# Kernel tuning notes

Measured on AMD Instinct MI355X. Metric: run time of the kernel, lower is better.

The kernel has to match this reference:

```python
import jax, jax.numpy as jnp
import numpy as np

PS = 8          # patch size
D_STATE = 16
D_CONV = 4
DT_RANK = 6     # ceil(96/16)
N_HEADS = 2
NEG = jnp.float32(-1e30)
_DIRS = np.array([[-1, 0], [1, 0], [0, -1], [0, 1]], np.int32)


def _ln(x, w, b, eps=1e-5):
    mu = x.mean(-1, keepdims=True)
    var = ((x - mu) ** 2).mean(-1, keepdims=True)
    return (x - mu) * jax.lax.rsqrt(var + eps) * w + b


def _vit_score_map(x, pos_embed, proj_w, proj_b, in_w, in_b, out_w, out_b,
                   ln1_w, ln1_b, ff1_w, ff1_b, ff2_w, ff2_b, ln2_w, ln2_b,
                   score_w, score_b):
    B, C, H, W = x.shape
    Hp, Wp = H // PS, W // PS
    N = Hp * Wp
    E = proj_w.shape[0]
    # F.unfold ordering: per patch the vector is (C, kr, kc) flattened
    patches = x.reshape(B, C, Hp, PS, Wp, PS).transpose(0, 2, 4, 1, 3, 5).reshape(B, N, C * PS * PS)
    patches = patches @ proj_w.T + proj_b
    if pos_embed.shape[1] != N:
        o = int(pos_embed.shape[1] ** 0.5)
        pe = jax.image.resize(pos_embed.reshape(1, o, o, E), (1, Hp, Wp, E), 'bilinear').reshape(1, N, E)
    else:
        pe = pos_embed
    patches = patches + 0.1 * pe
    # nn.TransformerEncoderLayer defaults: post-norm, ReLU, eval (no dropout)
    qkv = patches @ in_w.T + in_b
    q, k, v = jnp.split(qkv, 3, axis=-1)
    dh = E // N_HEADS
    def heads(t):
        return t.reshape(B, N, N_HEADS, dh).transpose(0, 2, 1, 3)
    q, k, v = heads(q), heads(k), heads(v)
    attn = jax.nn.softmax(jnp.einsum('bhqd,bhkd->bhqk', q, k) / np.float32(np.sqrt(dh)), axis=-1)
    ctx = jnp.einsum('bhqk,bhkd->bhqd', attn, v).transpose(0, 2, 1, 3).reshape(B, N, E)
    src = _ln(patches + (ctx @ out_w.T + out_b), ln1_w, ln1_b)
    ff = jax.nn.relu(src @ ff1_w.T + ff1_b) @ ff2_w.T + ff2_b
    src = _ln(src + ff, ln2_w, ln2_b)
    scores = jax.nn.sigmoid((src @ score_w.T + score_b)[..., 0])
    pvar = patches.var(axis=-1, ddof=1)          # torch.var is unbiased
    final = 0.7 * scores + 0.3 * jax.nn.sigmoid(pvar * 10.0)
    return final.reshape(B, Hp, Wp)


def _traversal(score):
    """Greedy adaptive patch traversal: start at global argmax, walk to the best
    unvisited 4-neighbor; on dead-end jump to the global argmax over unvisited."""
    Hp, Wp = score.shape
    n = Hp * Wp
    s = score.reshape(-1)
    dirs = jnp.asarray(_DIRS)
    start = jnp.argmax(s).astype(jnp.int32)
    visited0 = jnp.zeros((n,), bool).at[start].set(True)

    def step(carry, _):
        visited, cur = carry
        ci, cj = cur // Wp, cur % Wp
        ni, nj = ci + dirs[:, 0], cj + dirs[:, 1]
        valid = (ni >= 0) & (ni < Hp) & (nj >= 0) & (nj < Wp)
        nidx = (jnp.clip(ni, 0, Hp - 1) * Wp + jnp.clip(nj, 0, Wp - 1)).astype(jnp.int32)
        nsc = jnp.where(valid & ~visited[nidx], s[nidx], NEG)
        b = jnp.argmax(nsc)                       # first-max tie-break == '>' loop order
        jump = jnp.argmax(jnp.where(visited, NEG, s)).astype(jnp.int32)
        nxt = jnp.where(nsc[b] > NEG * 0.5, nidx[b], jump).astype(jnp.int32)
        return (visited.at[nxt].set(True), nxt), nxt

    _, rest = jax.lax.scan(step, (visited0, start), None, length=n - 1)
    return jnp.concatenate([start[None], rest])


def _mamba(u, in_w, conv_w, conv_b, xproj_w, dt_w, dt_b, A_log, D_skip, out_w):
    B, L, _ = u.shape
    d_in = conv_w.shape[0]
    xz = u @ in_w.T                               # (B,L,2*d_in)
    xx, z = jnp.split(xz, 2, axis=-1)
    # causal depthwise conv over sequence
    xc = jnp.pad(xx.transpose(0, 2, 1), ((0, 0), (0, 0), (D_CONV - 1, 0)))
    xc = jax.lax.conv_general_dilated(xc, conv_w, (1,), 'VALID',
                                      feature_group_count=d_in,
                                      dimension_numbers=('NCH', 'OIH', 'NCH'))
    xx = jax.nn.silu((xc + conv_b[None, :, None]).transpose(0, 2, 1))   # (B,L,d_in)
    dbl = xx @ xproj_w.T
    dt, Bm, Cm = jnp.split(dbl, [DT_RANK, DT_RANK + D_STATE], axis=-1)
    dt = jax.nn.softplus(dt @ dt_w.T + dt_b)      # (B,L,d_in)
    A = -jnp.exp(A_log)                           # (d_in, d_state)

    def step(h, inp):
        dt_t, B_t, C_t, x_t = inp                 # (B,d_in),(B,ds),(B,ds),(B,d_in)
        h = jnp.exp(dt_t[..., None] * A) * h + (dt_t * x_t)[..., None] * B_t[:, None, :]
        return h, jnp.einsum('bds,bs->bd', h, C_t)

    h0 = jnp.zeros((B, d_in, D_STATE), u.dtype)
    xs = (dt.transpose(1, 0, 2), Bm.transpose(1, 0, 2), Cm.transpose(1, 0, 2), xx.transpose(1, 0, 2))
    _, ys = jax.lax.scan(step, h0, xs)
    y = ys.transpose(1, 0, 2) + xx * D_skip
    return (y * jax.nn.silu(z)) @ out_w.T


def setup_inputs() -> dict:
    key = jax.random.key(0)
    ks = jax.random.split(key, 20)
    B, C, H, W = 2, 96, 128, 128
    E, FF = 96, 2048
    d_in, dr, ds, dc = 192, 6, 16, 4
    f32 = jnp.float32
    def w(k, shape, s=0.02):
        return jax.random.normal(k, shape, f32) * s
    return dict(
        x=jax.random.normal(ks[0], (B, C, H, W), f32),
        pe=w(ks[1], (B, H * W, C), 0.02),
        pos_embed=w(ks[2], (1, 784, E)),
        vit_proj_w=w(ks[3], (E, C * PS * PS)),
        vit_proj_b=jnp.zeros((E,), f32),
        attn_in_w=w(ks[4], (3 * E, E)),
        attn_in_b=jnp.zeros((3 * E,), f32),
        attn_out_w=w(ks[5], (E, E)),
        attn_out_b=jnp.zeros((E,), f32),
        ln1_w=jnp.ones((E,), f32), ln1_b=jnp.zeros((E,), f32),
        ff1_w=w(ks[6], (FF, E)), ff1_b=jnp.zeros((FF,), f32),
        ff2_w=w(ks[7], (E, FF)), ff2_b=jnp.zeros((E,), f32),
        ln2_w=jnp.ones((E,), f32), ln2_b=jnp.zeros((E,), f32),
        score_w=w(ks[8], (1, E)), score_b=jnp.zeros((1,), f32),
        norm_w=jnp.ones((C,), f32), norm_b=jnp.zeros((C,), f32),
        in_proj_w=w(ks[9], (2 * d_in, C)),
        conv_w=w(ks[10], (d_in, 1, dc), 0.1),
        conv_b=jnp.zeros((d_in,), f32),
        x_proj_w=w(ks[11], (dr + 2 * ds, d_in)),
        dt_w=w(ks[12], (d_in, dr)),
        dt_b=jnp.full((d_in,), -4.6, f32),        # softplus(dt_b) ~ 0.01 (mamba dt init)
        A_log=jnp.log(jnp.tile(jnp.arange(1, ds + 1, dtype=f32), (d_in, 1))),
        D_skip=jnp.ones((d_in,), f32),
        out_proj_w=w(ks[13], (C, d_in)),
    )


def reference(x, pe, pos_embed, vit_proj_w, vit_proj_b, attn_in_w, attn_in_b,
              attn_out_w, attn_out_b, ln1_w, ln1_b, ff1_w, ff1_b, ff2_w, ff2_b,
              ln2_w, ln2_b, score_w, score_b, norm_w, norm_b, in_proj_w,
              conv_w, conv_b, x_proj_w, dt_w, dt_b, A_log, D_skip, out_proj_w):
    B, C, H, W = x.shape
    n = H * W
    # Dynamic_Adaptive_Scan with the code's DCNv3Function-is-None fallback:
    # x = input_last, permuted back to channels-first => identity on x.
    x_adapted = x
    score_map = _vit_score_map(x_adapted, pos_embed, vit_proj_w, vit_proj_b,
                               attn_in_w, attn_in_b, attn_out_w, attn_out_b,
                               ln1_w, ln1_b, ff1_w, ff1_b, ff2_w, ff2_b,
                               ln2_w, ln2_b, score_w, score_b)
    order = jax.vmap(_traversal)(jax.lax.stop_gradient(score_map))    # (B, Hp*Wp)
    Hp, Wp = score_map.shape[1], score_map.shape[2]
    pi, pj = order // Wp, order % Wp
    # expand each patch into its PSxPS pixels in raster order
    offs = (jnp.arange(PS, dtype=jnp.int32)[:, None] * W + jnp.arange(PS, dtype=jnp.int32)[None, :]).reshape(-1)
    idx = ((pi * PS * W + pj * PS)[..., None] + offs).reshape(B, n)    # (B, n)
    x_tok = jnp.take_along_axis(x_adapted.reshape(B, C, n), idx[:, None, :], axis=2).transpose(0, 2, 1)
    pe_r = jnp.take_along_axis(pe, idx[..., None], axis=1)
    tokens = _ln(x_tok + pe_r, norm_w, norm_b)
    y = _mamba(tokens, in_proj_w, conv_w, conv_b, x_proj_w, dt_w, dt_b, A_log, D_skip, out_proj_w)
    # scatter back to spatial raster order
    out = jax.vmap(lambda yb, ib: jnp.zeros_like(yb).at[ib].set(yb))(y, idx)
    return out.transpose(0, 2, 1).reshape(B, C, H, W)
```

## Files before the change

### kernel.cpp

```cpp
#include <hip/hip_runtime.h>
#include <math.h>

#define BB 2
#define CC 96
#define HH 128
#define WW 128
#define PS 8
#define HP 16
#define WP 16
#define NPATCH 256
#define EE 96
#define FF 2048
#define DH 48
#define DIN 192
#define DR 6
#define DS 16
#define LL 16384
#define NCHUNK 512
#define CLEN 32
#define NSEG 16
#define SEGC 32
#define KTOT 6144
#define KSPLIT 32
#define KSL 192

__device__ __forceinline__ float sigmoid_acc(float x){ return 1.f/(1.f+expf(-x)); }
__device__ __forceinline__ float sigmoid_fast(float x){ return 1.f/(1.f+__expf(-x)); }

__global__ void k_resize_pe(const float* __restrict__ pos, float* __restrict__ pe16){
  int n = blockIdx.x;
  int oi = n / WP, oj = n % WP;
  int e = threadIdx.x;
  const float inv = 1.75f;
  float sfi = (oi + 0.5f)*inv - 0.5f;
  float sfj = (oj + 0.5f)*inv - 0.5f;
  int i0 = max(0, (int)ceilf(sfi - inv)), i1 = min(27, (int)floorf(sfi + inv));
  int j0 = max(0, (int)ceilf(sfj - inv)), j1 = min(27, (int)floorf(sfj + inv));
  float si = 0.f, sj = 0.f;
  for(int j=i0;j<=i1;j++) si += fmaxf(0.f, 1.f - fabsf(sfi - (float)j)/inv);
  for(int j=j0;j<=j1;j++) sj += fmaxf(0.f, 1.f - fabsf(sfj - (float)j)/inv);
  float acc = 0.f;
  for(int ji=i0;ji<=i1;ji++){
    float wv = fmaxf(0.f, 1.f - fabsf(sfi - (float)ji)/inv) / si;
    for(int jj=j0;jj<=j1;jj++){
      float wu = fmaxf(0.f, 1.f - fabsf(sfj - (float)jj)/inv);
      acc += wv * (wu/sj) * pos[(ji*28+jj)*EE + e];
    }
  }
  pe16[n*EE + e] = acc;
}

__global__ void k_wtr(const float* __restrict__ vw, float* __restrict__ Wt){
  __shared__ float t[64*97];
  int k0 = blockIdx.x*64;
  int tid = threadIdx.x;
  for(int i=tid;i<64*EE;i+=256){
    int e = i>>6, kk = i&63;
    t[kk*97 + e] = vw[(size_t)e*KTOT + k0 + kk];
  }
  __syncthreads();
  for(int i=tid;i<64*EE;i+=256){
    int kk = i/EE, e = i%EE;
    Wt[(size_t)(k0+kk)*EE + e] = t[kk*97 + e];
  }
}

__global__ __launch_bounds__(384) void k_pproj(const float* __restrict__ x,
    const float* __restrict__ Wt, float* __restrict__ part){
  __shared__ float As[16*196];
  int bidx = blockIdx.x;
  int ks = bidx & (KSPLIT-1);
  int pb = bidx >> 5;
  int b = pb >> 4, pi = pb & 15;
  int c0 = ks*3;
  int tid = threadIdx.x;
  for(int i=tid;i<24*128;i+=384){
    int row = i>>7;
    int col = i&127;
    int cl = row>>3, dr = row&7;
    float v = x[(((size_t)(b*CC + c0+cl))<<14) + (size_t)((pi*PS+dr)<<7) + col];
    As[(col>>3)*196 + cl*64 + dr*8 + (col&7)] = v;
  }
  __syncthreads();
  int e = tid % EE;
  int pq = tid / EE;
  const float* wp = Wt + (size_t)(ks*KSL)*EE + e;
  float acc0=0.f, acc1=0.f, acc2=0.f, acc3=0.f;
  const float4* A0 = (const float4*)(As + (pq*4+0)*196);
  const float4* A1 = (const float4*)(As + (pq*4+1)*196);
  const float4* A2 = (const float4*)(As + (pq*4+2)*196);
  const float4* A3 = (const float4*)(As + (pq*4+3)*196);
  #pragma unroll 4
  for(int k4=0;k4<48;k4++){
    float w0 = wp[(k4*4+0)*EE];
    float w1 = wp[(k4*4+1)*EE];
    float w2 = wp[(k4*4+2)*EE];
    float w3 = wp[(k4*4+3)*EE];
    float4 a;
    a = A0[k4]; acc0 += a.x*w0 + a.y*w1 + a.z*w2 + a.w*w3;
    a = A1[k4]; acc1 += a.x*w0 + a.y*w1 + a.z*w2 + a.w*w3;
    a = A2[k4]; acc2 += a.x*w0 + a.y*w1 + a.z*w2 + a.w*w3;
    a = A3[k4]; acc3 += a.x*w0 + a.y*w1 + a.z*w2 + a.w*w3;
  }
  size_t gp0 = (size_t)b*NPATCH + pi*WP + pq*4;
  part[((size_t)ks*512 + gp0+0)*EE + e] = acc0;
  part[((size_t)ks*512 + gp0+1)*EE + e] = acc1;
  part[((size_t)ks*512 + gp0+2)*EE + e] = acc2;
  part[((size_t)ks*512 + gp0+3)*EE + e] = acc3;
}

__global__ __launch_bounds__(320) void k_preduce_qkv(const float* __restrict__ part,
    const float* __restrict__ pb, const float* __restrict__ pe16,
    const float* __restrict__ inw, const float* __restrict__ inb,
    float* __restrict__ patches, float* __restrict__ pvar, float* __restrict__ qkv){
  int gp = blockIdx.x;
  int n = gp % NPATCH;
  int tid = threadIdx.x;
  __shared__ float a[EE];
  __shared__ float ps[2], pq2[2];
  float v = 0.f;
  if(tid < EE){
    float s = 0.f;
    #pragma unroll 8
    for(int ks=0;ks<KSPLIT;ks++) s += part[((size_t)ks*512 + gp)*EE + tid];
    v = s + pb[tid] + 0.1f*pe16[n*EE + tid];
    a[tid] = v;
    patches[(size_t)gp*EE + tid] = v;
  }
  if(tid < 128){
    float sv = v, sq = v*v;
    for(int off=32; off>0; off>>=1){ sv += __shfl_xor(sv, off); sq += __shfl_xor(sq, off); }
    if((tid&63)==0){ ps[tid>>6]=sv; pq2[tid>>6]=sq; }
  }
  __syncthreads();
  if(tid==0){
    float s = ps[0]+ps[1], qq = pq2[0]+pq2[1];
    float mu = s/EE;
    pvar[gp] = (qq - EE*mu*mu)/(EE-1);
  }
  if(tid < 288){
    const float4* ar = (const float4*)a;
    const float4* wr = (const float4*)(inw + (size_t)tid*EE);
    float4 s4 = {0.f,0.f,0.f,0.f};
    #pragma unroll
    for(int k=0;k<24;k++){
      float4 av=ar[k], wv=wr[k];
      s4.x += av.x*wv.x; s4.y += av.y*wv.y; s4.z += av.z*wv.z; s4.w += av.w*wv.w;
    }
    qkv[(size_t)gp*288 + tid] = inb[tid] + (s4.x+s4.y)+(s4.z+s4.w);
  }
}

__global__ void k_attn(const float* __restrict__ qkv, float* __restrict__ ctx){
  int gb = blockIdx.x;
  int i = gb % NPATCH; int h = (gb/NPATCH)&1; int b = gb/(NPATCH*2);
  int tid = threadIdx.x;
  __shared__ float q[DH];
  __shared__ float p[NPATCH];
  __shared__ float red[NPATCH];
  __shared__ float red2[4][DH];
  const float* base = qkv + (size_t)b*NPATCH*288;
  if(tid < DH) q[tid] = base[(size_t)i*288 + h*DH + tid];
  __syncthreads();
  float sc;
  {
    const float4* krow = (const float4*)(base + (size_t)tid*288 + 96 + h*DH);
    const float4* q4 = (const float4*)q;
    float4 s4 = {0.f,0.f,0.f,0.f};
    #pragma unroll
    for(int k=0;k<12;k++){
      float4 kv=krow[k], qv=q4[k];
      s4.x += qv.x*kv.x; s4.y += qv.y*kv.y; s4.z += qv.z*kv.z; s4.w += qv.w*kv.w;
    }
    sc = ((s4.x+s4.y)+(s4.z+s4.w)) * 0.14433756729740643f;
  }
  red[tid] = sc; __syncthreads();
  for(int st=128; st>0; st>>=1){ if(tid<st) red[tid]=fmaxf(red[tid],red[tid+st]); __syncthreads(); }
  float mx = red[0]; __syncthreads();
  float ev = expf(sc - mx);
  red[tid] = ev; __syncthreads();
  for(int st=128; st>0; st>>=1){ if(tid<st) red[tid]+=red[tid+st]; __syncthreads(); }
  float denom = red[0]; __syncthreads();
  p[tid] = ev/denom;
  __syncthreads();
  if(tid < 192){
    int jg = tid/DH, dd = tid%DH;
    const float* vb = base + 192 + h*DH + dd;
    float acc0 = 0.f, acc1 = 0.f;
    #pragma unroll 4
    for(int j=jg*64; j<jg*64+64; j+=2){
      acc0 += p[j]*vb[(size_t)j*288];
      acc1 += p[j+1]*vb[(size_t)(j+1)*288];
    }
    red2[jg][dd] = acc0+acc1;
  }
  __syncthreads();
  if(tid < DH){
    ctx[((size_t)b*NPATCH + i)*EE + h*DH + tid] =
      red2[0][tid]+red2[1][tid]+red2[2][tid]+red2[3][tid];
  }
}

__global__ void k_ln1(const float* __restrict__ ctx, const float* __restrict__ ow,
                      const float* __restrict__ ob, const float* __restrict__ patches,
                      const float* __restrict__ lw, const float* __restrict__ lb,
                      float* __restrict__ src1){
  int row = blockIdx.x; int tid = threadIdx.x;
  __shared__ float a[EE];
  __shared__ float ps[2], pq2[2], st[2];
  if(tid < EE) a[tid] = ctx[(size_t)row*EE + tid];
  __syncthreads();
  float o = 0.f;
  if(tid < EE){
    const float4* ar = (const float4*)a;
    const float4* wr = (const float4*)(ow + (size_t)tid*EE);
    float4 s4 = {0.f,0.f,0.f,0.f};
    #pragma unroll
    for(int k=0;k<24;k++){
      float4 av=ar[k], wv=wr[k];
      s4.x += av.x*wv.x; s4.y += av.y*wv.y; s4.z += av.z*wv.z; s4.w += av.w*wv.w;
    }
    o = ob[tid] + (s4.x+s4.y)+(s4.z+s4.w) + patches[(size_t)row*EE + tid];
  }
  float sv = o, sq = o*o;
  for(int off=32; off>0; off>>=1){ sv += __shfl_xor(sv, off); sq += __shfl_xor(sq, off); }
  if((tid&63)==0){ ps[tid>>6]=sv; pq2[tid>>6]=sq; }
  __syncthreads();
  if(tid==0){
    float s = ps[0]+ps[1], qq = pq2[0]+pq2[1];
    float mu = s/EE;
    st[0]=mu; st[1]=rsqrtf(qq/EE - mu*mu + 1e-5f);
  }
  __syncthreads();
  if(tid < EE) src1[(size_t)row*EE + tid] = (o-st[0])*st[1]*lw[tid] + lb[tid];
}

__global__ __launch_bounds__(512) void k_ff1(const float* __restrict__ src1,
    const float* __restrict__ w1, const float* __restrict__ b1, float* __restrict__ ffh){
  int row0 = blockIdx.x*2; int tid = threadIdx.x;
  const float4* a0 = (const float4*)(src1 + (size_t)row0*EE);
  const float4* a1 = (const float4*)(src1 + (size_t)(row0+1)*EE);
  for(int fo=0;fo<4;fo++){
    int f = fo*512 + tid;
    const float4* wr = (const float4*)(w1 + (size_t)f*EE);
    float bc = b1[f];
    float acc0=bc, acc1=bc;
    #pragma unroll
    for(int k=0;k<24;k++){
      float4 wv = wr[k];
      float4 av;
      av = a0[k]; acc0 += av.x*wv.x+av.y*wv.y+av.z*wv.z+av.w*wv.w;
      av = a1[k]; acc1 += av.x*wv.x+av.y*wv.y+av.z*wv.z+av.w*wv.w;
    }
    ffh[(size_t)(row0+0)*FF + f] = fmaxf(acc0, 0.f);
    ffh[(size_t)(row0+1)*FF + f] = fmaxf(acc1, 0.f);
  }
}

__global__ __launch_bounds__(384) void k_ff2(const float* __restrict__ ffh,
    const float* __restrict__ w2, const float* __restrict__ b2,
    const float* __restrict__ src1, float* __restrict__ src2){
  __shared__ float partl[8][EE];
  int row0 = blockIdx.x*2; int tid = threadIdx.x;
  int e = tid % EE, fg = tid / EE;
  const float4* wr = (const float4*)(w2 + (size_t)e*FF + fg*512);
  const float4* h0 = (const float4*)(ffh + (size_t)row0*FF + fg*512);
  const float4* h1 = (const float4*)(ffh + (size_t)(row0+1)*FF + fg*512);
  float acc0=0.f, acc1=0.f;
  #pragma unroll 4
  for(int k=0;k<128;k++){
    float4 wv = wr[k];
    float4 hv;
    hv = h0[k]; acc0 += hv.x*wv.x+hv.y*wv.y+hv.z*wv.z+hv.w*wv.w;
    hv = h1[k]; acc1 += hv.x*wv.x+hv.y*wv.y+hv.z*wv.z+hv.w*wv.w;
  }
  partl[0*4+fg][e] = acc0;
  partl[1*4+fg][e] = acc1;
  __syncthreads();
  if(tid < 192){
    int r = tid / EE, e2 = tid % EE;
    float s = partl[r*4+0][e2] + partl[r*4+1][e2] + partl[r*4+2][e2] + partl[r*4+3][e2];
    src2[(size_t)(row0+r)*EE + e2] = s + b2[e2] + src1[(size_t)(row0+r)*EE + e2];
  }
}

__global__ void k_ln2_score(const float* __restrict__ src2,
    const float* __restrict__ lw, const float* __restrict__ lb,
    const float* __restrict__ sw, const float* __restrict__ sb,
    const float* __restrict__ pvar, float* __restrict__ fscore){
  int row = blockIdx.x; int tid = threadIdx.x;
  float v = (tid < EE) ? src2[(size_t)row*EE + tid] : 0.f;
  float sv = v, sq = v*v;
  for(int off=32; off>0; off>>=1){ sv += __shfl_xor(sv, off); sq += __shfl_xor(sq, off); }
  __shared__ float ps[2], pq2[2], st[2];
  int wid = tid>>6;
  if((tid&63)==0){ ps[wid]=sv; pq2[wid]=sq; }
  __syncthreads();
  if(tid==0){
    float s = ps[0]+ps[1], qq = pq2[0]+pq2[1];
    float mu = s/EE;
    st[0]=mu; st[1]=rsqrtf(qq/EE - mu*mu + 1e-5f);
  }
  __syncthreads();
  float o = (tid < EE) ? ((v-st[0])*st[1]*lw[tid] + lb[tid]) * sw[tid] : 0.f;
  for(int off=32; off>0; off>>=1) o += __shfl_xor(o, off);
  if((tid&63)==0) ps[wid] = o;
  __syncthreads();
  if(tid==0){
    float acc = ps[0]+ps[1] + sb[0];
    fscore[row] = 0.7f*sigmoid_acc(acc) + 0.3f*sigmoid_acc(pvar[row]*10.f);
  }
}

__global__ void k_traversal(const float* __restrict__ fscore, int* __restrict__ order){
  int b = blockIdx.x; int lane = threadIdx.x;
  __shared__ float fsl[NPATCH];
  __shared__ int   sidxl[NPATCH];
  for(int k=lane;k<NPATCH;k+=64) fsl[k] = fscore[b*NPATCH+k];
  __syncthreads();
  {
    float s0=fsl[lane], s1=fsl[64+lane], s2=fsl[128+lane], s3=fsl[192+lane];
    int i0=lane, i1=64+lane, i2=128+lane, i3=192+lane;
    int c0=0,c1=0,c2=0,c3=0;
    for(int j=0;j<NPATCH;j++){
      float sj=fsl[j];
      c0 += (sj>s0 || (sj==s0 && j<i0)) ? 1:0;
      c1 += (sj>s1 || (sj==s1 && j<i1)) ? 1:0;
      c2 += (sj>s2 || (sj==s2 && j<i2)) ? 1:0;
      c3 += (sj>s3 || (sj==s3 && j<i3)) ? 1:0;
    }
    sidxl[c0]=i0; sidxl[c1]=i1; sidxl[c2]=i2; sidxl[c3]=i3;
  }
  __syncthreads();
  if(lane==0){
    int ptr = 0;
    int cur = sidxl[0];
    order[b*NPATCH] = cur;
    fsl[cur] = -1e30f;
    for(int step=1; step<NPATCH; step++){
      int ci = cur>>4, cj = cur&15;
      float n0 = (ci>0)  ? fsl[cur-16] : -1e30f;
      float n1 = (ci<15) ? fsl[cur+16] : -1e30f;
      float n2 = (cj>0)  ? fsl[cur-1]  : -1e30f;
      float n3 = (cj<15) ? fsl[cur+1]  : -1e30f;
      float bv = n0; int bi = cur-16;
      if(n1 > bv){ bv=n1; bi=cur+16; }
      if(n2 > bv){ bv=n2; bi=cur-1; }
      if(n3 > bv){ bv=n3; bi=cur+1; }
      int nxt;
      if(bv > -1e29f){
        nxt = bi;
      } else {
        while(fsl[sidxl[ptr]] <= -1e29f) ptr++;
        nxt = sidxl[ptr];
      }
      fsl[nxt] = -1e30f;
      order[b*NPATCH + step] = nxt;
      cur = nxt;
    }
  }
}

__global__ __launch_bounds__(256) void k_gather_ln(const float* __restrict__ x,
    const float* __restrict__ pe, const int* __restrict__ order,
    const float* __restrict__ nw, const float* __restrict__ nb,
    float* __restrict__ tokens){
  __shared__ float val[64*97];
  int gb = blockIdx.x; int b = gb >> 8; int r = gb & 255;
  int tid = threadIdx.x;
  int p = order[b*NPATCH + r]; int pi = p>>4, pj = p&15;
  for(int i=tid;i<96*64;i+=256){
    int c = i>>6, q = i&63;
    int dr = q>>3, dc = q&7;
    val[q*97 + c] = x[(((size_t)(b*CC + c))<<14) + (size_t)((pi*PS+dr)<<7) + pj*PS + dc];
  }
  __syncthreads();
  for(int i=tid;i<64*EE;i+=256){
    int q = i/EE, c = i%EE;
    int pix = ((pi*PS + (q>>3))<<7) + pj*PS + (q&7);
    val[q*97 + c] += pe[((size_t)b*(HH*WW) + pix)*CC + c];
  }
  __syncthreads();
  int wid = tid>>6, lane = tid&63;
  for(int t=wid; t<64; t+=4){
    float v1 = val[t*97 + lane];
    float v2 = (lane<32) ? val[t*97 + 64 + lane] : 0.f;
    float sv = v1+v2, sq = v1*v1 + v2*v2;
    for(int off=32; off>0; off>>=1){ sv += __shfl_xor(sv, off); sq += __shfl_xor(sq, off); }
    float mu = sv/EE;
    float rs = rsqrtf(sq/EE - mu*mu + 1e-5f);
    size_t tb = ((size_t)b*LL + r*64 + t)*EE;
    tokens[tb + lane] = (v1-mu)*rs*nw[lane] + nb[lane];
    if(lane < 32) tokens[tb + 64 + lane] = (v2-mu)*rs*nw[64+lane] + nb[64+lane];
  }
}

__global__ __launch_bounds__(768, 5) void k_inproj_conv(const float* __restrict__ tokens,
    const float* __restrict__ w, const float* __restrict__ cw, const float* __restrict__ cb,
    float* __restrict__ z, float* __restrict__ xc){
  __shared__ float a[35*EE];
  __shared__ float ps[12*384];
  __shared__ float xxl[35*DIN];
  int rb = blockIdx.x; size_t row0 = (size_t)rb*32;
  int l0 = (int)(row0 % LL);
  int tid = threadIdx.x;
  int kh = tid / 384;
  int col = tid - kh*384;
  {
    const float4* src = (const float4*)(tokens + (row0-3)*EE);
    float4* adst = (float4*)a;
    for(int idx=tid; idx<840; idx+=768){
      float4 v;
      if(l0==0 && idx<72){ v.x=0.f; v.y=0.f; v.z=0.f; v.w=0.f; }
      else v = src[idx];
      adst[idx] = v;
    }
  }
  float4 wv[12];
  const float4* wr4 = (const float4*)(w + (size_t)col*EE + kh*48);
  #pragma unroll
  for(int i=0;i<12;i++) wv[i] = wr4[i];
  __syncthreads();
  #pragma unroll
  for(int g=0; g<3; g++){
    float acc[12];
    #pragma unroll
    for(int r=0;r<12;r++){
      int gi = g*12 + r;
      if(gi < 35){
        const float4* ar = (const float4*)(a + gi*EE + kh*48);
        float4 s4 = {0.f,0.f,0.f,0.f};
        #pragma unroll
        for(int i=0;i<12;i++){
          float4 av = ar[i];
          s4.x += av.x*wv[i].x; s4.y += av.y*wv[i].y; s4.z += av.z*wv[i].z; s4.w += av.w*wv[i].w;
        }
        acc[r] = (s4.x+s4.y)+(s4.z+s4.w);
      } else acc[r] = 0.f;
    }
    if(kh==1){
      #pragma unroll
      for(int r=0;r<12;r++) if(g*12+r < 35) ps[r*384 + col] = acc[r];
    }
    __syncthreads();
    if(kh==0){
      #pragma unroll
      for(int r=0;r<12;r++){
        int gi = g*12 + r;
        if(gi < 35){
          float tot = acc[r] + ps[r*384 + col];
          if(col < DIN) xxl[gi*DIN + col] = tot;
          else if(gi >= 3) z[(row0 + gi - 3)*DIN + (col - DIN)] = tot;
        }
      }
    }
    __syncthreads();
  }
  #pragma unroll
  for(int it=0; it<8; it++){
    int idx = tid + it*768;
    int rr = idx / DIN, d = idx - rr*DIN;
    float v = cb[d]
      + cw[d*4+0]*xxl[(rr+0)*DIN + d]
      + cw[d*4+1]*xxl[(rr+1)*DIN + d]
      + cw[d*4+2]*xxl[(rr+2)*DIN + d]
      + cw[d*4+3]*xxl[(rr+3)*DIN + d];
    xc[(row0 + rr)*DIN + d] = v * sigmoid_fast(v);
  }
}

__global__ __launch_bounds__(320) void k_xproj(const float* __restrict__ xc, const float* __restrict__ xpw,
    const float* __restrict__ dtw, const float* __restrict__ dtb,
    float* __restrict__ dt, float* __restrict__ Bm, float* __restrict__ Cm){
  __shared__ float a[8][196];
  __shared__ float dbl[8][40];
  int rb = blockIdx.x; size_t row0 = (size_t)rb*8;
  int tid = threadIdx.x;
  for(int i=tid;i<8*DIN;i+=320){ int r=i/DIN, k=i%DIN; a[r][k] = xc[(row0+r)*DIN + k]; }
  __syncthreads();
  {
    int r = tid & 7, o = tid >> 3;
    if(o < 38){
      const float4* wr = (const float4*)(xpw + (size_t)o*DIN);
      const float4* ar = (const float4*)(a[r]);
      float4 s4 = {0.f,0.f,0.f,0.f};
      #pragma unroll
      for(int k=0;k<48;k++){
        float4 av=ar[k], wv=wr[k];
        s4.x += av.x*wv.x; s4.y += av.y*wv.y; s4.z += av.z*wv.z; s4.w += av.w*wv.w;
      }
      dbl[r][o] = (s4.x+s4.y)+(s4.z+s4.w);
    }
  }
  __syncthreads();
  for(int t=tid;t<8*DIN;t+=320){
    int r = t/DIN, d = t%DIN;
    float acc = dtb[d];
    #pragma unroll
    for(int j=0;j<DR;j++) acc += dbl[r][j]*dtw[d*DR+j];
    dt[(row0+r)*DIN + d] = fmaxf(acc, 0.f) + log1pf(__expf(-fabsf(acc)));
  }
  if(tid < 8*DS){
    int r = tid/DS, s = tid%DS;
    Bm[(row0+r)*DS + s] = dbl[r][6+s];
    Cm[(row0+r)*DS + s] = dbl[r][22+s];
  }
}

__global__ __launch_bounds__(192) void k_scan1(const float* __restrict__ dt,
    const float* __restrict__ xc, const float* __restrict__ Bm,
    const float* __restrict__ Alog, float* __restrict__ hend, float* __restrict__ sumdt){
  int blk = blockIdx.x;
  int b = blk >> 9, c = blk & (NCHUNK-1);
  int d = threadIdx.x;
  float A[16];
  {
    const float4* a4 = (const float4*)(Alog + d*DS);
    #pragma unroll
    for(int i=0;i<4;i++){
      float4 v = a4[i];
      A[i*4+0]=-expf(v.x); A[i*4+1]=-expf(v.y); A[i*4+2]=-expf(v.z); A[i*4+3]=-expf(v.w);
    }
  }
  float h[16];
  #pragma unroll
  for(int s=0;s<16;s++) h[s]=0.f;
  float sd = 0.f;
  size_t base = (size_t)b*LL + (size_t)c*CLEN;
  const float* dp = dt + base*DIN + d;
  const float* xp = xc + base*DIN + d;
  const float4* bp = (const float4*)(Bm + base*DS);
  for(int t=0;t<CLEN;t++){
    float dtv = dp[(size_t)t*DIN];
    float xv  = xp[(size_t)t*DIN];
    float4 b0=bp[t*4+0], b1=bp[t*4+1], b2=bp[t*4+2], b3=bp[t*4+3];
    float e[16];
    #pragma unroll
    for(int s=0;s<16;s++) e[s] = __expf(dtv*A[s]);
    float Bv[16] = {b0.x,b0.y,b0.z,b0.w,b1.x,b1.y,b1.z,b1.w,b2.x,b2.y,b2.z,b2.w,b3.x,b3.y,b3.z,b3.w};
    float dx = dtv*xv; sd += dtv;
    #pragma unroll
    for(int s=0;s<16;s++) h[s] = e[s]*h[s] + dx*Bv[s];
  }
  size_t o = ((size_t)c*BB + b)*DIN + d;
  float4* hp = (float4*)(hend + o*DS);
  hp[0] = make_float4(h[0],h[1],h[2],h[3]);
  hp[1] = make_float4(h[4],h[5],h[6],h[7]);
  hp[2] = make_float4(h[8],h[9],h[10],h[11]);
  hp[3] = make_float4(h[12],h[13],h[14],h[15]);
  sumdt[o] = sd;
}

__global__ __launch_bounds__(256) void k_scan2a(const float* __restrict__ hend,
    const float* __restrict__ sumdt, const float* __restrict__ Alog,
    float* __restrict__ segP, float* __restrict__ segH){
  int g = blockIdx.x*256 + threadIdx.x;
  int seg = g / 6144; int r = g % 6144;
  int b = r / 3072; int d = (r % 3072) >> 4; int s = r & 15;
  float A = -expf(Alog[d*DS + s]);
  float P = 1.f, H = 0.f;
  int c0 = seg*SEGC;
  for(int cc=0; cc<SEGC; cc+=4){
    float sd[4], he[4];
    #pragma unroll
    for(int j=0;j<4;j++){
      size_t o = ((size_t)(c0+cc+j)*BB + b)*DIN + d;
      sd[j] = sumdt[o]; he[j] = hend[o*DS + s];
    }
    #pragma unroll
    for(int j=0;j<4;j++){
      float aa = __expf(A*sd[j]);
      H = aa*H + he[j]; P *= aa;
    }
  }
  segP[seg*6144 + r] = P; segH[seg*6144 + r] = H;
}

__global__ void k_scan2b(const float* __restrict__ segP, const float* __restrict__ segH,
                         float* __restrict__ segHin){
  int r = blockIdx.x*256 + threadIdx.x;
  float P[NSEG], H[NSEG];
  #pragma unroll
  for(int sg=0; sg<NSEG; sg++){ P[sg]=segP[sg*6144+r]; H[sg]=segH[sg*6144+r]; }
  float h = 0.f;
  #pragma unroll
  for(int sg=0; sg<NSEG; sg++){
    segHin[sg*6144 + r] = h;
    h = P[sg]*h + H[sg];
  }
}

__global__ __launch_bounds__(256) void k_scan2c(float* __restrict__ hend,
    const float* __restrict__ sumdt, const float* __restrict__ Alog,
    const float* __restrict__ segHin){
  int g = blockIdx.x*256 + threadIdx.x;
  int seg = g / 6144; int r = g % 6144;
  int b = r / 3072; int d = (r % 3072) >> 4; int s = r & 15;
  float A = -expf(Alog[d*DS + s]);
  float h = segHin[seg*6144 + r];
  int c0 = seg*SEGC;
  for(int cc=0; cc<SEGC; cc+=4){
    float sd[4], he[4]; size_t oo[4];
    #pragma unroll
    for(int j=0;j<4;j++){
      oo[j] = ((size_t)(c0+cc+j)*BB + b)*DIN + d;
      sd[j] = sumdt[oo[j]]; he[j] = hend[oo[j]*DS + s];
    }
    #pragma unroll
    for(int j=0;j<4;j++){
      hend[oo[j]*DS + s] = h;
      float aa = __expf(A*sd[j]);
      h = aa*h + he[j];
    }
  }
}

__global__ __launch_bounds__(192) void k_scan3(const float* __restrict__ dt,
    const float* __restrict__ xc, const float* __restrict__ Bm, const float* __restrict__ Cm,
    const float* __restrict__ Alog, const float* __restrict__ hin,
    const float* __restrict__ Dskip, float* __restrict__ zg){
  int blk = blockIdx.x;
  int b = blk >> 9, c = blk & (NCHUNK-1);
  int d = threadIdx.x;
  float A[16];
  {
    const float4* a4 = (const float4*)(Alog + d*DS);
    #pragma unroll
    for(int i=0;i<4;i++){
      float4 v = a4[i];
      A[i*4+0]=-expf(v.x); A[i*4+1]=-expf(v.y); A[i*4+2]=-expf(v.z); A[i*4+3]=-expf(v.w);
    }
  }
  size_t o = ((size_t)c*BB + b)*DIN + d;
  float h[16];
  {
    const float4* hi = (const float4*)(hin + o*DS);
    #pragma unroll
    for(int i=0;i<4;i++){
      float4 v = hi[i];
      h[i*4+0]=v.x; h[i*4+1]=v.y; h[i*4+2]=v.z; h[i*4+3]=v.w;
    }
  }
  float Dv = Dskip[d];
  size_t base = (size_t)b*LL + (size_t)c*CLEN;
  const float* dp = dt + base*DIN + d;
  const float* xp = xc + base*DIN + d;
  float* zp = zg + base*DIN + d;
  const float4* bp = (const float4*)(Bm + base*DS);
  const float4* cp = (const float4*)(Cm + base*DS);
  for(int t=0;t<CLEN;t++){
    float dtv = dp[(size_t)t*DIN];
    float xv  = xp[(size_t)t*DIN];
    float zv  = zp[(size_t)t*DIN];
    float4 b0=bp[t*4+0], b1=bp[t*4+1], b2=bp[t*4+2], b3=bp[t*4+3];
    float4 c0=cp[t*4+0], c1=cp[t*4+1], c2=cp[t*4+2], c3=cp[t*4+3];
    float e[16];
    #pragma unroll
    for(int s=0;s<16;s++) e[s] = __expf(dtv*A[s]);
    float Bv[16] = {b0.x,b0.y,b0.z,b0.w,b1.x,b1.y,b1.z,b1.w,b2.x,b2.y,b2.z,b2.w,b3.x,b3.y,b3.z,b3.w};
    float Cv[16] = {c0.x,c0.y,c0.z,c0.w,c1.x,c1.y,c1.z,c1.w,c2.x,c2.y,c2.z,c2.w,c3.x,c3.y,c3.z,c3.w};
    float dx = dtv*xv;
    float y = 0.f;
    #pragma unroll
    for(int s=0;s<16;s++){ h[s] = e[s]*h[s] + dx*Bv[s]; y += h[s]*Cv[s]; }
    float yy = y + xv*Dv;
    zp[(size_t)t*DIN] = yy * (zv * sigmoid_fast(zv));
  }
}

__global__ __launch_bounds__(192) void k_outproj(const float* __restrict__ g,
    const float* __restrict__ w, float* __restrict__ ytok){
  __shared__ float ps[32*100];
  int rb = blockIdx.x; size_t row0 = (size_t)rb*32;
  int tid = threadIdx.x;
  int col = tid % EE, kh = tid / EE;
  float4 wv[24];
  const float4* wr4 = (const float4*)(w + (size_t)col*DIN + kh*96);
  #pragma unroll
  for(int i=0;i<24;i++) wv[i] = wr4[i];
  float acc[32];
  for(int r=0;r<32;r++){
    const float4* ar = (const float4*)(g + (row0+r)*DIN + kh*96);
    float4 s4 = {0.f,0.f,0.f,0.f};
    #pragma unroll
    for(int i=0;i<24;i++){
      float4 av=ar[i];
      s4.x += av.x*wv[i].x; s4.y += av.y*wv[i].y; s4.z += av.z*wv[i].z; s4.w += av.w*wv[i].w;
    }
    acc[r] = (s4.x+s4.y)+(s4.z+s4.w);
  }
  if(kh==1){
    #pragma unroll
    for(int r=0;r<32;r++) ps[r*100+col] = acc[r];
  }
  __syncthreads();
  if(kh==0){
    #pragma unroll
    for(int r=0;r<32;r++) ytok[(row0+r)*EE + col] = acc[r] + ps[r*100+col];
  }
}

__global__ __launch_bounds__(256) void k_scatter(const float* __restrict__ ytok,
    const int* __restrict__ order, float* __restrict__ out){
  __shared__ float yt[64*100];
  int gb = blockIdx.x; int b = gb>>8, r = gb&255;
  int p = order[b*NPATCH + r]; int pi = p>>4, pj = p&15;
  int tid = threadIdx.x;
  for(int i=tid;i<64*24;i+=256){
    int q = i/24, c4 = i%24;
    float4 v = ((const float4*)(ytok + ((size_t)b*LL + r*64 + q)*EE))[c4];
    ((float4*)(yt + q*100))[c4] = v;
  }
  __syncthreads();
  int q = tid&63; int cg = tid>>6;
  int pix = ((pi*PS + (q>>3))<<7) + pj*PS + (q&7);
  for(int c=cg;c<CC;c+=4){
    out[(((size_t)(b*CC + c))<<14) + pix] = yt[q*100 + c];
  }
}

extern "C" void kernel_launch(void* const* d_in, const int* in_sizes, int n_in,
                              void* d_out, int out_size, void* d_ws, size_t ws_size,
                              hipStream_t stream){
  (void)in_sizes; (void)n_in; (void)out_size; (void)ws_size;
  const float* x    = (const float*)d_in[0];
  const float* pe   = (const float*)d_in[1];
  const float* pos  = (const float*)d_in[2];
  const float* vw   = (const float*)d_in[3];
  const float* vb   = (const float*)d_in[4];
  const float* inw  = (const float*)d_in[5];
  const float* inb  = (const float*)d_in[6];
  const float* ow   = (const float*)d_in[7];
  const float* ob   = (const float*)d_in[8];
  const float* l1w  = (const float*)d_in[9];
  const float* l1b  = (const float*)d_in[10];
  const float* f1w  = (const float*)d_in[11];
  const float* f1b  = (const float*)d_in[12];
  const float* f2w  = (const float*)d_in[13];
  const float* f2b  = (const float*)d_in[14];
  const float* l2w  = (const float*)d_in[15];
  const float* l2b  = (const float*)d_in[16];
  const float* sw   = (const float*)d_in[17];
  const float* sb   = (const float*)d_in[18];
  const float* nw   = (const float*)d_in[19];
  const float* nb   = (const float*)d_in[20];
  const float* ipw  = (const float*)d_in[21];
  const float* cw   = (const float*)d_in[22];
  const float* cb   = (const float*)d_in[23];
  const float* xpw  = (const float*)d_in[24];
  const float* dtw  = (const float*)d_in[25];
  const float* dtbp = (const float*)d_in[26];
  const float* alog = (const float*)d_in[27];
  const float* dsk  = (const float*)d_in[28];
  const float* opw  = (const float*)d_in[29];
  float* out = (float*)d_out;

  char* wsb = (char*)d_ws;
  size_t off = 0;
  auto alloc = [&](size_t nfloats)->void*{
    void* p = (void*)(wsb + off);
    off += ((nfloats*sizeof(float) + 255) & ~(size_t)255);
    return p;
  };
  float* pe16    = (float*)alloc(256*96);
  float* patches = (float*)alloc(512*96);
  float* pvar    = (float*)alloc(512);
  float* qkv     = (float*)alloc((size_t)512*288);
  float* ctxb    = (float*)alloc(512*96);
  float* src1    = (float*)alloc(512*96);
  float* ffh     = (float*)alloc((size_t)512*2048);
  float* fscore  = (float*)alloc(512);
  int*   order   = (int*)  alloc(512);
  float* tokens  = (float*)alloc((size_t)2*16384*96);
  float* xxb     = (float*)alloc((size_t)2*16384*192);
  float* zb      = (float*)alloc((size_t)2*16384*192);
  float* xcb     = (float*)alloc((size_t)2*16384*192);
  float* Bmat    = (float*)alloc((size_t)2*16384*16);
  float* Cmat    = (float*)alloc((size_t)2*16384*16);
  float* sumdt   = (float*)alloc((size_t)NCHUNK*2*192);
  float* segP    = (float*)alloc((size_t)NSEG*6144);
  float* segH    = (float*)alloc((size_t)NSEG*6144);
  float* segHin  = (float*)alloc((size_t)NSEG*6144);
  float* dtbuf = xxb;
  float* Wt    = xxb;
  float* part  = tokens;
  float* hend  = tokens;
  float* hin   = hend;
  float* ytok  = tokens;
  float* src2  = qkv;

  k_resize_pe   <<<256,   96, 0, stream>>>(pos, pe16);
  k_wtr         <<<96,   256, 0, stream>>>(vw, Wt);
  k_pproj       <<<1024, 384, 0, stream>>>(x, Wt, part);
  k_preduce_qkv <<<512,  320, 0, stream>>>(part, vb, pe16, inw, inb, patches, pvar, qkv);
  k_attn        <<<1024, 256, 0, stream>>>(qkv, ctxb);
  k_ln1         <<<512,  128, 0, stream>>>(ctxb, ow, ob, patches, l1w, l1b, src1);
  k_ff1         <<<256,  512, 0, stream>>>(src1, f1w, f1b, ffh);
  k_ff2         <<<256,  384, 0, stream>>>(ffh, f2w, f2b, src1, src2);
  k_ln2_score   <<<512,  128, 0, stream>>>(src2, l2w, l2b, sw, sb, pvar, fscore);
  k_traversal   <<<2,     64, 0, stream>>>(fscore, order);
  k_gather_ln   <<<512,  256, 0, stream>>>(x, pe, order, nw, nb, tokens);
  k_inproj_conv <<<1024, 768, 0, stream>>>(tokens, ipw, cw, cb, zb, xcb);
  k_xproj       <<<4096, 320, 0, stream>>>(xcb, xpw, dtw, dtbp, dtbuf, Bmat, Cmat);
  k_scan1       <<<1024, 192, 0, stream>>>(dtbuf, xcb, Bmat, alog, hend, sumdt);
  k_scan2a      <<<384,  256, 0, stream>>>(hend, sumdt, alog, segP, segH);
  k_scan2b      <<<24,   256, 0, stream>>>(segP, segH, segHin);
  k_scan2c      <<<384,  256, 0, stream>>>(hend, sumdt, alog, segHin);
  k_scan3       <<<1024, 192, 0, stream>>>(dtbuf, xcb, Bmat, Cmat, alog, hin, dsk, zb);
  k_outproj     <<<1024, 192, 0, stream>>>(zb, opw, ytok);
  k_scatter     <<<512,  256, 0, stream>>>(ytok, order, out);
}
```

Before: 533.9 us.

## Speculate traversal jump target and split outproj K four ways with LDS-staged rows

The serial traversal loop now reads neighbour scores through clamped addresses without branches, and keeps a precomputed next global-argmax candidate so a dead end needs no search inside the loop. The Mamba output projection now handles 16 rows per block with 384 threads, stages the activation rows in shared memory, splits the reduction dimension four ways and combines the partials through LDS. This aims to shorten the single-lane critical path and raise parallelism in the projection, at the cost of extra barriers and twice as many blocks.

```diff
diff --git a/kernel.cpp b/kernel.cpp
--- a/kernel.cpp
+++ b/kernel.cpp
@@ -333,30 +333,33 @@
   }
   __syncthreads();
   if(lane==0){
-    int ptr = 0;
     int cur = sidxl[0];
     order[b*NPATCH] = cur;
     fsl[cur] = -1e30f;
+    int ptr = 1;
+    int jcand = sidxl[1];
     for(int step=1; step<NPATCH; step++){
       int ci = cur>>4, cj = cur&15;
-      float n0 = (ci>0)  ? fsl[cur-16] : -1e30f;
-      float n1 = (ci<15) ? fsl[cur+16] : -1e30f;
-      float n2 = (cj>0)  ? fsl[cur-1]  : -1e30f;
-      float n3 = (cj<15) ? fsl[cur+1]  : -1e30f;
-      float bv = n0; int bi = cur-16;
-      if(n1 > bv){ bv=n1; bi=cur+16; }
-      if(n2 > bv){ bv=n2; bi=cur-1; }
-      if(n3 > bv){ bv=n3; bi=cur+1; }
-      int nxt;
-      if(bv > -1e29f){
-        nxt = bi;
-      } else {
-        while(fsl[sidxl[ptr]] <= -1e29f) ptr++;
-        nxt = sidxl[ptr];
-      }
+      int a0 = (ci>0)  ? cur-16 : cur;
+      int a1 = (ci<15) ? cur+16 : cur;
+      int a2 = (cj>0)  ? cur-1  : cur;
+      int a3 = (cj<15) ? cur+1  : cur;
+      float n0 = fsl[a0];
+      float n1 = fsl[a1];
+      float n2 = fsl[a2];
+      float n3 = fsl[a3];
+      float bv = n0; int bi = a0;
+      if(n1 > bv){ bv=n1; bi=a1; }
+      if(n2 > bv){ bv=n2; bi=a2; }
+      if(n3 > bv){ bv=n3; bi=a3; }
+      int nxt = (bv > -1e29f) ? bi : jcand;
       fsl[nxt] = -1e30f;
       order[b*NPATCH + step] = nxt;
       cur = nxt;
+      if(nxt == jcand && step < NPATCH-1){
+        float jv;
+        do { ptr++; jcand = sidxl[ptr]; jv = fsl[jcand]; } while(jv <= -1e29f);
+      }
     }
   }
 }
@@ -668,35 +671,56 @@
   }
 }
 
-__global__ __launch_bounds__(192) void k_outproj(const float* __restrict__ g,
+__global__ __launch_bounds__(384) void k_outproj(const float* __restrict__ g,
     const float* __restrict__ w, float* __restrict__ ytok){
-  __shared__ float ps[32*100];
-  int rb = blockIdx.x; size_t row0 = (size_t)rb*32;
+  __shared__ float a[16*DIN];
+  __shared__ float psA[16*EE];
+  __shared__ float psB[16*EE];
+  int rb = blockIdx.x; size_t row0 = (size_t)rb*16;
   int tid = threadIdx.x;
-  int col = tid % EE, kh = tid / EE;
-  float4 wv[24];
-  const float4* wr4 = (const float4*)(w + (size_t)col*DIN + kh*96);
+  int col = tid % EE, kq = tid / EE;
+  {
+    const float4* src = (const float4*)(g + row0*DIN);
+    float4* ad = (float4*)a;
+    ad[tid] = src[tid];
+    ad[tid+384] = src[tid+384];
+  }
+  float4 wv[12];
+  const float4* wr4 = (const float4*)(w + (size_t)col*DIN + kq*48);
   #pragma unroll
-  for(int i=0;i<24;i++) wv[i] = wr4[i];
-  float acc[32];
-  for(int r=0;r<32;r++){
-    const float4* ar = (const float4*)(g + (row0+r)*DIN + kh*96);
+  for(int i=0;i<12;i++) wv[i] = wr4[i];
+  __syncthreads();
+  float acc[16];
+  for(int r=0;r<16;r++){
+    const float4* ar = (const float4*)(a + r*DIN + kq*48);
     float4 s4 = {0.f,0.f,0.f,0.f};
     #pragma unroll
-    for(int i=0;i<24;i++){
-      float4 av=ar[i];
+    for(int i=0;i<12;i++){
+      float4 av = ar[i];
       s4.x += av.x*wv[i].x; s4.y += av.y*wv[i].y; s4.z += av.z*wv[i].z; s4.w += av.w*wv[i].w;
     }
     acc[r] = (s4.x+s4.y)+(s4.z+s4.w);
   }
-  if(kh==1){
-    #pragma unroll
-    for(int r=0;r<32;r++) ps[r*100+col] = acc[r];
-  }
-  __syncthreads();
-  if(kh==0){
-    #pragma unroll
-    for(int r=0;r<32;r++) ytok[(row0+r)*EE + col] = acc[r] + ps[r*100+col];
+  if(kq==1){
+    for(int r=0;r<16;r++) psA[r*EE+col] = acc[r];
+  }
+  if(kq==3){
+    for(int r=0;r<16;r++) psB[r*EE+col] = acc[r];
+  }
+  __syncthreads();
+  if(kq==0){
+    for(int r=0;r<16;r++) acc[r] += psA[r*EE+col];
+  }
+  if(kq==2){
+    for(int r=0;r<16;r++) acc[r] += psB[r*EE+col];
+  }
+  __syncthreads();
+  if(kq==2){
+    for(int r=0;r<16;r++) psA[r*EE+col] = acc[r];
+  }
+  __syncthreads();
+  if(kq==0){
+    for(int r=0;r<16;r++) ytok[(row0+r)*EE + col] = acc[r] + psA[r*EE+col];
   }
 }
 
@@ -807,6 +831,6 @@
   k_scan2b      <<<24,   256, 0, stream>>>(segP, segH, segHin);
   k_scan2c      <<<384,  256, 0, stream>>>(hend, sumdt, alog, segHin);
   k_scan3       <<<1024, 192, 0, stream>>>(dtbuf, xcb, Bmat, Cmat, alog, hin, dsk, zb);
-  k_outproj     <<<1024, 192, 0, stream>>>(zb, opw, ytok);
+  k_outproj     <<<2048, 384, 0, stream>>>(zb, opw, ytok);
   k_scatter     <<<512,  256, 0, stream>>>(ytok, order, out);
 }
```

New measurement: 506.4 us. 1.05x faster.
